# Performance work log

Hardware: AMD Instinct MI355X
Metric: run time of the kernel (lower is better)

The kernel has to match this reference:

```python
import jax, jax.numpy as jnp
import numpy as np
jax.config.update("jax_enable_x64", True)

TAPS, DELAY = 5, 3
EPS = 1e-6        # DNN_WPE.eps: power clamp before WPE
WPE_EPS = 1e-10   # wpe_one_iteration eps: inverse-power clamp + diag loading


def _signal_framing(Y, L):
    # Y: (..., T) -> (..., T-L+1, L) sliding frames (as_strided equivalent)
    T = Y.shape[-1]
    idx = jnp.arange(T - L + 1)[:, None] + jnp.arange(L)[None, :]
    return Y[..., idx]


def _wpe_one_iteration(Y, power, taps, delay):
    # Y: (B,F,C,T) complex128, power: (B,F,T) float64
    B, F, C, T = Y.shape
    inv_power = 1.0 / jnp.maximum(power, WPE_EPS)
    Tp = T - delay - taps + 1
    # tap-stacked delayed signal, taps axis reversed: (B,F,C,Tp,taps)
    Psi = _signal_framing(Y, taps)[..., :Tp, :][..., ::-1]
    Psi_n = Psi.conj() * inv_power[:, :, None, delay + taps - 1:, None]
    # covariance R: (B,F,taps*C,taps*C); cross-corr P: (B,F,taps,C_e,C_d)
    R = jnp.einsum("bfdtk,bfetl->bfkdle", Psi_n, Psi).reshape(B, F, taps * C, taps * C)
    P = jnp.einsum("bfdtk,bfet->bfked", Psi_n, Y[..., delay + taps - 1:])
    # v: (B,F,C_e,taps*C_d); conj filter G = inv(R) @ v^T  (X = v @ inv(R)^T)
    v = P.transpose(0, 1, 3, 2, 4).reshape(B, F, C, taps * C)
    eye = jnp.eye(taps * C, dtype=R.dtype)
    tr = jnp.trace(R, axis1=-2, axis2=-1).real[..., None, None] / (taps * C)
    G = jnp.linalg.solve(R + WPE_EPS * tr * eye, v.transpose(0, 1, 3, 2))
    G = G.reshape(B, F, taps, C, C)  # (B,F,tau,d,e) conjugated filter matrix
    # reverb tail: sum over taps of filtered, delayed signal
    tail = jnp.zeros_like(Y)
    for tau in range(taps):  # taps=5, small fixed loop
        s = delay + tau
        contrib = jnp.einsum("bfde,bfdt->bfet", G[:, :, tau], Y[..., : T - s])
        tail = tail.at[..., s:].add(contrib)
    return Y - tail


def setup_inputs() -> dict:
    key = jax.random.key(0)
    k1, k2, k3 = jax.random.split(key, 3)
    B, T, C, F = 4, 512, 8, 257
    data_real = jax.random.normal(k1, (B, T, C, F), dtype=jnp.float32)
    data_imag = jax.random.normal(k2, (B, T, C, F), dtype=jnp.float32)
    ilens = jax.random.randint(k3, (B,), 256, T + 1)
    return {"data_real": data_real, "data_imag": data_imag, "ilens": ilens}


def reference(data_real, data_imag, ilens):
    # (B,T,C,F) -> (B,F,C,T)
    data = (data_real + 1j * data_imag).transpose(0, 3, 2, 1)
    # power averaged over channels, clamped (B,F,T)
    power = jnp.maximum(jnp.mean(data.real ** 2 + data.imag ** 2, axis=-2), EPS)
    enh = _wpe_one_iteration(data.astype(jnp.complex128), power.astype(jnp.float64), TAPS, DELAY)
    enh = enh.astype(jnp.complex64)
    T = enh.shape[-1]
    pad = (jnp.arange(T)[None, :] >= ilens[:, None])[:, None, None, :]  # (B,1,1,T)
    enh = jnp.where(pad, 0.0 + 0.0j, enh)
    enh = enh.transpose(0, 3, 2, 1)  # back to (B,T,C,F)
    return enh.real, enh.imag, power
```

## Files before the change

kernel.cpp:

```cpp
#include <hip/hip_runtime.h>
#include <hip/hip_fp16.h>

#define B_ 4
#define T_ 512
#define C_ 8
#define F_ 257
#define TAPS 5
#define DELAY 3
#define N_ 40
#define NA 48
#define TP 505
#define T0 7
#define BF (B_*F_)
#define BTCF ((size_t)B_*T_*C_*F_)
#define YSH 532
#define YPAD 8
#define ZSD 20

typedef _Float16 half8 __attribute__((ext_vector_type(8)));
typedef float floatx4 __attribute__((ext_vector_type(4)));
typedef uint32_t uint32x4 __attribute__((ext_vector_type(4)));

__device__ inline uint32_t h2mul(uint32_t a, uint32_t b) {
    __half2 r = __hmul2(__builtin_bit_cast(__half2, a), __builtin_bit_cast(__half2, b));
    return __builtin_bit_cast(uint32_t, r);
}
__device__ inline uint32_t packf16(float2 v) {
    __half2 h = __floats2half2_rn(v.x, v.y);
    return __builtin_bit_cast(uint32_t, h);
}
__device__ inline float2 unpackf16(uint32_t u) {
    __half2 h = __builtin_bit_cast(__half2, u);
    return make_float2(__low2float(h), __high2float(h));
}
__device__ inline half8 mkfrag(uint32_t a, uint32_t b, uint32_t c, uint32_t d) {
    uint32x4 v = {a, b, c, d};
    return __builtin_bit_cast(half8, v);
}
__device__ inline int rowoff(int i) {
    return i * 49 - ((i * (i - 1)) >> 1);
}
__device__ inline int swz_w(int bid) {
    int xcd = bid & 7, slot = bid >> 3;
    return (xcd < 4) ? xcd * 129 + slot : 516 + (xcd - 4) * 128 + slot;
}

struct Frag { half8 X; half8 Y; };

__device__ inline Frag build2(const uint32_t* p, uint32_t sw0, uint32_t sw1,
                              uint32_t sw2, uint32_t sw3) {
    uint32_t q0 = p[0], q1 = p[1], q2 = p[2], q3 = p[3];
    uint32_t q4 = p[4], q5 = p[5], q6 = p[6], q7 = p[7];
    uint32_t x0 = __builtin_amdgcn_perm(q1, q0, 0x05040100);
    uint32_t y0 = __builtin_amdgcn_perm(q1, q0, 0x07060302);
    uint32_t x1 = __builtin_amdgcn_perm(q3, q2, 0x05040100);
    uint32_t y1 = __builtin_amdgcn_perm(q3, q2, 0x07060302);
    uint32_t x2 = __builtin_amdgcn_perm(q5, q4, 0x05040100);
    uint32_t y2 = __builtin_amdgcn_perm(q5, q4, 0x07060302);
    uint32_t x3 = __builtin_amdgcn_perm(q7, q6, 0x05040100);
    uint32_t y3 = __builtin_amdgcn_perm(q7, q6, 0x07060302);
    Frag f;
    f.X = mkfrag(h2mul(x0, sw0), h2mul(x1, sw1), h2mul(x2, sw2), h2mul(x3, sw3));
    f.Y = mkfrag(h2mul(y0, sw0), h2mul(y1, sw1), h2mul(y2, sw2), h2mul(y3, sw3));
    return f;
}
__device__ inline int zs_off(int j) {
    return (j < N_) ? (j & 7) * YSH + (YPAD + 4 - (j >> 3)) : (j - N_) * YSH + (YPAD + T0);
}

__global__ __launch_bounds__(256) void k_stage(const float* __restrict__ in_re,
                                               const float* __restrict__ in_im,
                                               uint32_t* __restrict__ Yh) {
    __shared__ uint32_t tile[32][33];
    int ft = blockIdx.x % 9;
    int tt = blockIdx.x / 9;
    int c = blockIdx.y, b = blockIdx.z;
    int tx = threadIdx.x, ty = threadIdx.y;
    int f = ft * 32 + tx;
#pragma unroll
    for (int i = 0; i < 4; ++i) {
        int t = tt * 32 + ty + i * 8;
        if (f < F_) {
            size_t idx = ((size_t)(b * T_ + t) * C_ + c) * F_ + f;
            tile[ty + i * 8][tx] = packf16(make_float2(in_re[idx], in_im[idx]));
        }
    }
    __syncthreads();
    int t2 = tt * 32 + tx;
#pragma unroll
    for (int i = 0; i < 4; ++i) {
        int f2 = ft * 32 + ty + i * 8;
        if (f2 < F_) {
            Yh[((size_t)(b * F_ + f2) * C_ + c) * T_ + t2] = tile[tx][ty + i * 8];
        }
    }
}

__global__ __launch_bounds__(256) void k_gramsolve(const uint32_t* __restrict__ Yh,
                                                   float2* __restrict__ Gbuf,
                                                   float* __restrict__ pow_out) {
    __shared__ uint32_t sYh[C_ * YSH];
    __shared__ __align__(16) uint32_t pool[3256];
    float* sPow = (float*)pool;
    uint32_t* sw_pk = pool + 640;
    float2* sAugU = (float2*)(pool + 896);
    int tid = threadIdx.x;

    int w = swz_w(blockIdx.x);

    {
        const uint32_t* ys = Yh + (size_t)w * (C_ * T_);
#pragma unroll 4
        for (int k = 0; k < 16; ++k) {
            int idx = tid + k * 256;
            int c = idx >> 9, t = idx & 511;
            sYh[c * YSH + YPAD + t] = ys[idx];
        }
        if (tid < 20) {
            int z = (tid < 8) ? tid : (512 + tid);
#pragma unroll
            for (int c = 0; c < C_; ++c) sYh[c * YSH + z] = 0;
        }
    }
    __syncthreads();

    {
        int t0 = tid, t1 = tid + 256;
        float s0 = 0.f, s1 = 0.f;
#pragma unroll
        for (int c = 0; c < C_; ++c) {
            float2 a0 = unpackf16(sYh[c * YSH + YPAD + t0]);
            float2 a1 = unpackf16(sYh[c * YSH + YPAD + t1]);
            s0 += a0.x * a0.x + a0.y * a0.y;
            s1 += a1.x * a1.x + a1.y * a1.y;
        }
        s0 = fmaxf(s0 * (1.0f / C_), 1e-6f);
        s1 = fmaxf(s1 * (1.0f / C_), 1e-6f);
        pow_out[(size_t)w * T_ + t0] = s0;
        pow_out[(size_t)w * T_ + t1] = s1;
        sPow[t0] = s0;
        sPow[t1] = s1;
    }
    __syncthreads();

    {
        int k0 = 2 * tid, k1 = k0 + 1;
        float w0 = (k0 < TP) ? rsqrtf(sPow[k0 + T0]) : 0.f;
        float w1 = (k1 < TP) ? rsqrtf(sPow[k1 + T0]) : 0.f;
        sw_pk[tid] = packf16(make_float2(w0, w1));
    }
    __syncthreads();

    int wv = tid >> 6, ln = tid & 63;
    int kg = ln >> 4;
    if (wv < 3) {
        int r16 = ln & 15;
        int offB = zs_off(wv * 16 + r16);
#pragma unroll 1
        for (int mt = 0; mt < 3; ++mt) {
            int offA = zs_off(mt * 16 + r16);
            floatx4 aRe = {0.f, 0.f, 0.f, 0.f};
            floatx4 aIm = {0.f, 0.f, 0.f, 0.f};
#pragma unroll 2
            for (int ks = 0; ks < 16; ++ks) {
                int kbase = ks * 32 + kg * 8;
                uint32x4 sv = *(const uint32x4*)&sw_pk[kbase >> 1];
                Frag B = build2(&sYh[offB + kbase], sv[0], sv[1], sv[2], sv[3]);
                Frag A = build2(&sYh[offA + kbase], sv[0], sv[1], sv[2], sv[3]);
                half8 nYa = -A.Y;
                aRe = __builtin_amdgcn_mfma_f32_16x16x32_f16(A.X, B.X, aRe, 0, 0, 0);
                aRe = __builtin_amdgcn_mfma_f32_16x16x32_f16(A.Y, B.Y, aRe, 0, 0, 0);
                aIm = __builtin_amdgcn_mfma_f32_16x16x32_f16(A.X, B.Y, aIm, 0, 0, 0);
                aIm = __builtin_amdgcn_mfma_f32_16x16x32_f16(nYa, B.X, aIm, 0, 0, 0);
            }
#pragma unroll
            for (int r = 0; r < 4; ++r) {
                int m = mt * 16 + kg * 4 + r;
                int col = wv * 16 + r16;
                if (m < N_ && col >= m)
                    sAugU[rowoff(m) + col - m] = make_float2(aRe[r], aIm[r]);
            }
        }
    }
    __syncthreads();

    if (tid < 64) {
        float dv = (tid < N_) ? sAugU[rowoff(tid)].x : 0.f;
#pragma unroll
        for (int off = 32; off; off >>= 1) dv += __shfl_xor(dv, off, 64);
        if (tid < N_) sAugU[rowoff(tid)].x += 1e-10f * dv / N_;
    }
    __syncthreads();

    {
        int ri = tid >> 4, ci = tid & 15;
        float2 dq0, dq1, dq2;
#pragma unroll 1
        for (int p = 0; p < N_ - 2; p += 2) {
            if (p > 0 && ri == 0) {
                int qm = p - 1, roqm = rowoff(qm);
                if (ci < NA - qm)      sAugU[roqm + ci] = dq0;
                if (ci + 16 < NA - qm) sAugU[roqm + ci + 16] = dq1;
                if (ci + 32 < NA - qm) sAugU[roqm + ci + 32] = dq2;
            }
            int q = p + 1;
            int rop = rowoff(p), roq = rowoff(q);
            float2 Upp = sAugU[rop];
            float2 Upq = sAugU[rop + 1];
            float2 Uqq = sAugU[roq];
            float dn0 = Upp.x * Upp.x + Upp.y * Upp.y;
            float i0x = Upp.x / dn0, i0y = -Upp.y / dn0;
            float mqx = Upq.x * i0x + Upq.y * i0y;
            float mqy = Upq.x * i0y - Upq.y * i0x;
            float d1x = Uqq.x - (mqx * Upq.x - mqy * Upq.y);
            float d1y = Uqq.y - (mqx * Upq.y + mqy * Upq.x);
            float dn1 = d1x * d1x + d1y * d1y;
            float i1x = d1x / dn1, i1y = -d1y / dn1;
#pragma unroll 1
            for (int i = q + ri; i < N_; i += 16) {
                if (i == q) {
#pragma unroll
                    for (int s = 0; s < 3; ++s) {
                        int j = q + ci + 16 * s;
                        float2 r = make_float2(0.f, 0.f);
                        if (j < NA) {
                            float2 Upj = sAugU[rop + j - p];
                            float2 Uqj = sAugU[roq + j - q];
                            r.x = Uqj.x - (mqx * Upj.x - mqy * Upj.y);
                            r.y = Uqj.y - (mqx * Upj.y + mqy * Upj.x);
                        }
                        if (s == 0) dq0 = r; else if (s == 1) dq1 = r; else dq2 = r;
                    }
                } else {
                    float2 Upi = sAugU[rop + i - p];
                    float m0x = Upi.x * i0x + Upi.y * i0y;
                    float m0y = Upi.x * i0y - Upi.y * i0x;
                    float2 Uqi = sAugU[roq + i - q];
                    float ax = Uqi.x - (m0x * Upq.x - m0y * Upq.y);
                    float ay = -Uqi.y - (m0x * Upq.y + m0y * Upq.x);
                    float m1x = ax * i1x - ay * i1y;
                    float m1y = ax * i1y + ay * i1x;
                    int roi = rowoff(i) - i;
#pragma unroll 1
                    for (int j = i + ci; j < NA; j += 16) {
                        float2 Upj = sAugU[rop + j - p];
                        float2 Uqj = sAugU[roq + j - q];
                        float u1x = Uqj.x - (mqx * Upj.x - mqy * Upj.y);
                        float u1y = Uqj.y - (mqx * Upj.y + mqy * Upj.x);
                        float2 v = sAugU[roi + j];
                        v.x -= (m0x * Upj.x - m0y * Upj.y) + (m1x * u1x - m1y * u1y);
                        v.y -= (m0x * Upj.y + m0y * Upj.x) + (m1x * u1y + m1y * u1x);
                        sAugU[roi + j] = v;
                    }
                }
            }
            __syncthreads();
        }
        {
            int p = N_ - 2;
            if (ri == 0) {
                int qm = p - 1, roqm = rowoff(qm);
                if (ci < NA - qm)      sAugU[roqm + ci] = dq0;
                if (ci + 16 < NA - qm) sAugU[roqm + ci + 16] = dq1;
                if (ci + 32 < NA - qm) sAugU[roqm + ci + 32] = dq2;
            }
            int rop = rowoff(p);
            float2 piv = sAugU[rop];
            float dn = piv.x * piv.x + piv.y * piv.y;
            float px = piv.x / dn, py = -piv.y / dn;
#pragma unroll 1
            for (int i = p + 1 + ri; i < N_; i += 16) {
                float2 api = sAugU[rop + i - p];
                float mx = api.x * px + api.y * py;
                float my = api.x * py - api.y * px;
                int roi = rowoff(i) - i;
#pragma unroll 1
                for (int j = i + ci; j < NA; j += 16) {
                    float2 apj = sAugU[rop + j - p];
                    float2 v = sAugU[roi + j];
                    v.x -= mx * apj.x - my * apj.y;
                    v.y -= mx * apj.y + my * apj.x;
                    sAugU[roi + j] = v;
                }
            }
            __syncthreads();
        }
    }
    {
        int bc = tid & 7, br = tid >> 3;
        float2 defv = make_float2(0.f, 0.f);
        int defRow = -1;
#pragma unroll 1
        for (int p = N_ - 1; p >= 3; p -= 2) {
            if (defRow >= 0 && br == (defRow & 31))
                sAugU[rowoff(defRow) + N_ + bc - defRow] = defv;
            int q = p - 1;
            int rop = rowoff(p), roq = rowoff(q);
            float2 pivP = sAugU[rop];
            float dnP = pivP.x * pivP.x + pivP.y * pivP.y;
            float pPx = pivP.x / dnP, pPy = -pivP.y / dnP;
            float2 rhsP = sAugU[rop + N_ + bc - p];
            float xPx = rhsP.x * pPx - rhsP.y * pPy;
            float xPy = rhsP.x * pPy + rhsP.y * pPx;
            float2 pivQ = sAugU[roq];
            float dnQ = pivQ.x * pivQ.x + pivQ.y * pivQ.y;
            float pQx = pivQ.x / dnQ, pQy = -pivQ.y / dnQ;
            float2 Uqp = sAugU[roq + 1];
            float2 rhsQ = sAugU[roq + N_ + bc - q];
            float rqx = rhsQ.x - (Uqp.x * xPx - Uqp.y * xPy);
            float rqy = rhsQ.y - (Uqp.x * xPy + Uqp.y * xPx);
            float xQx = rqx * pQx - rqy * pQy;
            float xQy = rqx * pQy + rqy * pQx;
#pragma unroll 1
            for (int i = br; i <= p - 2; i += 32) {
                int roi = rowoff(i) - i;
                float2 Uip = sAugU[roi + p];
                float2 Uiq = sAugU[roi + q];
                float2 v = sAugU[roi + N_ + bc];
                v.x -= (Uip.x * xPx - Uip.y * xPy) + (Uiq.x * xQx - Uiq.y * xQy);
                v.y -= (Uip.x * xPy + Uip.y * xPx) + (Uiq.x * xQy + Uiq.y * xQx);
                sAugU[roi + N_ + bc] = v;
            }
            if (br == (q & 31)) defv = make_float2(rqx, rqy);
            defRow = q;
            __syncthreads();
        }
        {
            if (defRow >= 0 && br == (defRow & 31))
                sAugU[rowoff(defRow) + N_ + bc - defRow] = defv;
            int rop = rowoff(1);
            float2 piv = sAugU[rop];
            float dn = piv.x * piv.x + piv.y * piv.y;
            float px = piv.x / dn, py = -piv.y / dn;
            float2 rhs = sAugU[rop + N_ + bc - 1];
            float xr = rhs.x * px - rhs.y * py;
            float xi = rhs.x * py + rhs.y * px;
            if (br == 0) {
                float2 aip = sAugU[1];
                float2 v = sAugU[N_ + bc];
                v.x -= aip.x * xr - aip.y * xi;
                v.y -= aip.x * xi + aip.y * xr;
                sAugU[N_ + bc] = v;
            }
            __syncthreads();
        }
    }
    for (int idx = tid; idx < N_ * C_; idx += 256) {
        int j = idx >> 3;
        int e = idx & 7;
        int roj = rowoff(j);
        float2 piv = sAugU[roj];
        float dnm = piv.x * piv.x + piv.y * piv.y;
        float pix = piv.x / dnm, piy = -piv.y / dnm;
        float2 rhs = sAugU[roj + N_ + e - j];
        Gbuf[(size_t)w * (N_ * C_) + idx] =
            make_float2(rhs.x * pix - rhs.y * piy, rhs.x * piy + rhs.y * pix);
    }
}

__global__ __launch_bounds__(256) void k_tail(const uint32_t* __restrict__ Yh,
                                              const float2* __restrict__ Gbuf,
                                              const int* __restrict__ ilens,
                                              float* __restrict__ out_re,
                                              float* __restrict__ out_im) {
    __shared__ __align__(16) uint32_t zRe[64 * ZSD];
    __shared__ __align__(16) uint32_t zIm[64 * ZSD];
    int w = swz_w(blockIdx.x);
    int half = blockIdx.y;
    int b = w / F_;
    int f = w - b * F_;
    int ilen = ilens[b];
    const uint32_t* yw = Yh + (size_t)w * (C_ * T_);
    const float2* gw = Gbuf + (size_t)w * (N_ * C_);
    int tid = threadIdx.x;
    int wv = tid >> 6, ln = tid & 63, kg = ln >> 4;

    half8 aFr[2], aFi[2];
    {
        int m = ln & 15;
#pragma unroll
        for (int ks = 0; ks < 2; ++ks) {
            half8 hr = {}, hi = {};
#pragma unroll
            for (int q = 0; q < 8; ++q) {
                int j = ks * 32 + kg * 8 + q;
                float gx = 0.f, gy = 0.f;
                if (m < 8 && j < N_) {
                    float2 g = gw[j * 8 + m];
                    gx = g.x; gy = g.y;
                }
                hr[q] = (_Float16)gx;
                hi[q] = (_Float16)gy;
            }
            aFr[ks] = hr;
            aFi[ks] = hi;
        }
    }

    int trow = wv * 16 + (ln & 15);
#pragma unroll 1
    for (int ch = 0; ch < 4; ++ch) {
        int c0 = half * 256 + ch * 64;
        for (int idx = tid; idx < 1280; idx += 256) {
            int jp = idx >> 6, tl = idx & 63;
            int j0 = 2 * jp, j1 = j0 + 1;
            int s0 = c0 + tl - 3 - (j0 >> 3);
            uint32_t y0 = 0, y1 = 0;
            if (s0 >= 0) {
                y0 = yw[(j0 & 7) * T_ + s0];
                y1 = yw[(j1 & 7) * T_ + s0];
            }
            zRe[tl * ZSD + jp] = __builtin_amdgcn_perm(y1, y0, 0x05040100);
            zIm[tl * ZSD + jp] = __builtin_amdgcn_perm(y1, y0, 0x07060302);
        }
        __syncthreads();
        floatx4 accR = {0.f, 0.f, 0.f, 0.f};
        floatx4 accI = {0.f, 0.f, 0.f, 0.f};
        {
            int o0 = trow * ZSD + kg * 4;
            half8 Br0 = __builtin_bit_cast(half8, *(const uint32x4*)&zRe[o0]);
            half8 Bi0 = __builtin_bit_cast(half8, *(const uint32x4*)&zIm[o0]);
            half8 Br1 = {}, Bi1 = {};
            if (kg == 0) {
                int o1 = trow * ZSD + 16;
                Br1 = __builtin_bit_cast(half8, *(const uint32x4*)&zRe[o1]);
                Bi1 = __builtin_bit_cast(half8, *(const uint32x4*)&zIm[o1]);
            }
            half8 nFi0 = -aFi[0], nFi1 = -aFi[1];
            accR = __builtin_amdgcn_mfma_f32_16x16x32_f16(aFr[0], Br0, accR, 0, 0, 0);
            accR = __builtin_amdgcn_mfma_f32_16x16x32_f16(aFr[1], Br1, accR, 0, 0, 0);
            accI = __builtin_amdgcn_mfma_f32_16x16x32_f16(aFi[0], Br0, accI, 0, 0, 0);
            accI = __builtin_amdgcn_mfma_f32_16x16x32_f16(aFi[1], Br1, accI, 0, 0, 0);
            accR = __builtin_amdgcn_mfma_f32_16x16x32_f16(nFi0, Bi0, accR, 0, 0, 0);
            accR = __builtin_amdgcn_mfma_f32_16x16x32_f16(nFi1, Bi1, accR, 0, 0, 0);
            accI = __builtin_amdgcn_mfma_f32_16x16x32_f16(aFr[0], Bi0, accI, 0, 0, 0);
            accI = __builtin_amdgcn_mfma_f32_16x16x32_f16(aFr[1], Bi1, accI, 0, 0, 0);
        }
        if (kg < 2) {
            int tg = c0 + trow;
            bool dead = (tg >= ilen);
#pragma unroll
            for (int r = 0; r < 4; ++r) {
                int e = kg * 4 + r;
                float2 cf = unpackf16(yw[e * T_ + tg]);
                float ex = cf.x - accR[r];
                float ey = cf.y - accI[r];
                if (dead) { ex = 0.f; ey = 0.f; }
                size_t o = (size_t)b * T_ * C_ * F_ + ((size_t)tg * C_ + e) * F_ + f;
                out_re[o] = ex;
                out_im[o] = ey;
            }
        }
        __syncthreads();
    }
}

extern "C" void kernel_launch(void* const* d_in, const int* in_sizes, int n_in,
                              void* d_out, int out_size, void* d_ws, size_t ws_size,
                              hipStream_t stream) {
    const float* in_re = (const float*)d_in[0];
    const float* in_im = (const float*)d_in[1];
    const int* ilens = (const int*)d_in[2];

    float* out_re = (float*)d_out;
    float* out_im = out_re + BTCF;
    float* out_pw = out_im + BTCF;

    uint32_t* Yh = (uint32_t*)d_ws;
    float2* Gbuf = (float2*)(Yh + (size_t)BF * C_ * T_);

    dim3 tb(32, 8);
    dim3 tg(9 * 16, C_, B_);
    k_stage<<<tg, tb, 0, stream>>>(in_re, in_im, Yh);
    k_gramsolve<<<BF, 256, 0, stream>>>(Yh, Gbuf, out_pw);
    k_tail<<<dim3(BF, 2), 256, 0, stream>>>(Yh, Gbuf, ilens, out_re, out_im);
}
```

Before: 221.1 us.

## Fuse gram/solve and tail kernels into one per-bin kernel with staged K-slices

Merges the gram+solve kernel and the tail-filter kernel into a single kernel per (batch,freq) bin, keeping the solved filter in shared memory instead of round-tripping through a global buffer. The Gram matrix build is restructured: instead of caching the whole 8x512 signal in LDS and re-permuting fragments per MFMA, it stages pre-weighted, de-interleaved X/Y fragments for 128-sample slices into LDS, then runs all three row tiles per wave with register accumulators. This cuts LDS footprint, a kernel launch and the G buffer traffic. In exchange, the tail stage loses its 2-way split across blocks, so each block does twice the tail work serially and parallelism halves for that phase.

```diff
diff --git a/kernel.cpp b/kernel.cpp
--- a/kernel.cpp
+++ b/kernel.cpp
@@ -13,9 +13,8 @@
 #define T0 7
 #define BF (B_*F_)
 #define BTCF ((size_t)B_*T_*C_*F_)
-#define YSH 532
-#define YPAD 8
 #define ZSD 20
+#define PRS 68
 
 typedef _Float16 half8 __attribute__((ext_vector_type(8)));
 typedef float floatx4 __attribute__((ext_vector_type(4)));
@@ -33,39 +32,12 @@
     __half2 h = __builtin_bit_cast(__half2, u);
     return make_float2(__low2float(h), __high2float(h));
 }
-__device__ inline half8 mkfrag(uint32_t a, uint32_t b, uint32_t c, uint32_t d) {
-    uint32x4 v = {a, b, c, d};
-    return __builtin_bit_cast(half8, v);
-}
 __device__ inline int rowoff(int i) {
     return i * 49 - ((i * (i - 1)) >> 1);
 }
 __device__ inline int swz_w(int bid) {
     int xcd = bid & 7, slot = bid >> 3;
     return (xcd < 4) ? xcd * 129 + slot : 516 + (xcd - 4) * 128 + slot;
-}
-
-struct Frag { half8 X; half8 Y; };
-
-__device__ inline Frag build2(const uint32_t* p, uint32_t sw0, uint32_t sw1,
-                              uint32_t sw2, uint32_t sw3) {
-    uint32_t q0 = p[0], q1 = p[1], q2 = p[2], q3 = p[3];
-    uint32_t q4 = p[4], q5 = p[5], q6 = p[6], q7 = p[7];
-    uint32_t x0 = __builtin_amdgcn_perm(q1, q0, 0x05040100);
-    uint32_t y0 = __builtin_amdgcn_perm(q1, q0, 0x07060302);
-    uint32_t x1 = __builtin_amdgcn_perm(q3, q2, 0x05040100);
-    uint32_t y1 = __builtin_amdgcn_perm(q3, q2, 0x07060302);
-    uint32_t x2 = __builtin_amdgcn_perm(q5, q4, 0x05040100);
-    uint32_t y2 = __builtin_amdgcn_perm(q5, q4, 0x07060302);
-    uint32_t x3 = __builtin_amdgcn_perm(q7, q6, 0x05040100);
-    uint32_t y3 = __builtin_amdgcn_perm(q7, q6, 0x07060302);
-    Frag f;
-    f.X = mkfrag(h2mul(x0, sw0), h2mul(x1, sw1), h2mul(x2, sw2), h2mul(x3, sw3));
-    f.Y = mkfrag(h2mul(y0, sw0), h2mul(y1, sw1), h2mul(y2, sw2), h2mul(y3, sw3));
-    return f;
-}
-__device__ inline int zs_off(int j) {
-    return (j < N_) ? (j & 7) * YSH + (YPAD + 4 - (j >> 3)) : (j - N_) * YSH + (YPAD + T0);
 }
 
 __global__ __launch_bounds__(256) void k_stage(const float* __restrict__ in_re,
@@ -96,41 +68,34 @@
     }
 }
 
-__global__ __launch_bounds__(256) void k_gramsolve(const uint32_t* __restrict__ Yh,
-                                                   float2* __restrict__ Gbuf,
-                                                   float* __restrict__ pow_out) {
-    __shared__ uint32_t sYh[C_ * YSH];
-    __shared__ __align__(16) uint32_t pool[3256];
+__global__ __launch_bounds__(256) void k_compute(const uint32_t* __restrict__ Yh,
+                                                 const int* __restrict__ ilens,
+                                                 float* __restrict__ out_re,
+                                                 float* __restrict__ out_im,
+                                                 float* __restrict__ pow_out) {
+    __shared__ __align__(16) uint32_t pool[7296];
     float* sPow = (float*)pool;
-    uint32_t* sw_pk = pool + 640;
-    float2* sAugU = (float2*)(pool + 896);
+    uint32_t* sw_pk = pool + 512;
+    uint32_t* zX = pool + 768;
+    uint32_t* zY = pool + 768 + 48 * PRS;
+    float2* sAugU = (float2*)(pool + 768);
+    uint32_t* zRe = pool + 4032;
+    uint32_t* zIm = pool + 4032 + 64 * ZSD;
     int tid = threadIdx.x;
 
     int w = swz_w(blockIdx.x);
-
-    {
-        const uint32_t* ys = Yh + (size_t)w * (C_ * T_);
-#pragma unroll 4
-        for (int k = 0; k < 16; ++k) {
-            int idx = tid + k * 256;
-            int c = idx >> 9, t = idx & 511;
-            sYh[c * YSH + YPAD + t] = ys[idx];
-        }
-        if (tid < 20) {
-            int z = (tid < 8) ? tid : (512 + tid);
-#pragma unroll
-            for (int c = 0; c < C_; ++c) sYh[c * YSH + z] = 0;
-        }
-    }
-    __syncthreads();
+    int b = w / F_;
+    int f = w - b * F_;
+    int ilen = ilens[b];
+    const uint32_t* yw = Yh + (size_t)w * (C_ * T_);
 
     {
         int t0 = tid, t1 = tid + 256;
         float s0 = 0.f, s1 = 0.f;
 #pragma unroll
         for (int c = 0; c < C_; ++c) {
-            float2 a0 = unpackf16(sYh[c * YSH + YPAD + t0]);
-            float2 a1 = unpackf16(sYh[c * YSH + YPAD + t1]);
+            float2 a0 = unpackf16(yw[c * T_ + t0]);
+            float2 a1 = unpackf16(yw[c * T_ + t1]);
             s0 += a0.x * a0.x + a0.y * a0.y;
             s1 += a1.x * a1.x + a1.y * a1.y;
         }
@@ -152,34 +117,99 @@
     __syncthreads();
 
     int wv = tid >> 6, ln = tid & 63;
-    int kg = ln >> 4;
+    int kg = ln >> 4, r16 = ln & 15;
+    floatx4 aRe0 = {0.f, 0.f, 0.f, 0.f}, aIm0 = {0.f, 0.f, 0.f, 0.f};
+    floatx4 aRe1 = {0.f, 0.f, 0.f, 0.f}, aIm1 = {0.f, 0.f, 0.f, 0.f};
+    floatx4 aRe2 = {0.f, 0.f, 0.f, 0.f}, aIm2 = {0.f, 0.f, 0.f, 0.f};
+#pragma unroll 1
+    for (int sl = 0; sl < 4; ++sl) {
+#pragma unroll
+        for (int rep = 0; rep < 3; ++rep) {
+            int task = tid + rep * 256;
+            int j = task >> 4, g = task & 15;
+            int c = (j < N_) ? (j & 7) : (j - N_);
+            int sh = (j < N_) ? (4 - (j >> 3)) : 7;
+            int base = sl * 128 + g * 8 + sh;
+            const uint32_t* yc = yw + c * T_;
+            uint32_t q0 = yc[(base + 0 < 512) ? base + 0 : 511];
+            uint32_t q1 = yc[(base + 1 < 512) ? base + 1 : 511];
+            uint32_t q2 = yc[(base + 2 < 512) ? base + 2 : 511];
+            uint32_t q3 = yc[(base + 3 < 512) ? base + 3 : 511];
+            uint32_t q4 = yc[(base + 4 < 512) ? base + 4 : 511];
+            uint32_t q5 = yc[(base + 5 < 512) ? base + 5 : 511];
+            uint32_t q6 = yc[(base + 6 < 512) ? base + 6 : 511];
+            uint32_t q7 = yc[(base + 7 < 512) ? base + 7 : 511];
+            uint32x4 sv = *(const uint32x4*)&sw_pk[(sl * 128 + g * 8) >> 1];
+            uint32_t x0 = __builtin_amdgcn_perm(q1, q0, 0x05040100);
+            uint32_t y0 = __builtin_amdgcn_perm(q1, q0, 0x07060302);
+            uint32_t x1 = __builtin_amdgcn_perm(q3, q2, 0x05040100);
+            uint32_t y1 = __builtin_amdgcn_perm(q3, q2, 0x07060302);
+            uint32_t x2 = __builtin_amdgcn_perm(q5, q4, 0x05040100);
+            uint32_t y2 = __builtin_amdgcn_perm(q5, q4, 0x07060302);
+            uint32_t x3 = __builtin_amdgcn_perm(q7, q6, 0x05040100);
+            uint32_t y3 = __builtin_amdgcn_perm(q7, q6, 0x07060302);
+            uint32x4 vx = {h2mul(x0, sv[0]), h2mul(x1, sv[1]),
+                           h2mul(x2, sv[2]), h2mul(x3, sv[3])};
+            uint32x4 vy = {h2mul(y0, sv[0]), h2mul(y1, sv[1]),
+                           h2mul(y2, sv[2]), h2mul(y3, sv[3])};
+            *(uint32x4*)&zX[j * PRS + g * 4] = vx;
+            *(uint32x4*)&zY[j * PRS + g * 4] = vy;
+        }
+        __syncthreads();
+        if (wv < 3) {
+            int rowB = wv * 16 + r16;
+#pragma unroll
+            for (int l = 0; l < 4; ++l) {
+                int off = l * 16 + kg * 4;
+                half8 BX = __builtin_bit_cast(half8, *(const uint32x4*)&zX[rowB * PRS + off]);
+                half8 BY = __builtin_bit_cast(half8, *(const uint32x4*)&zY[rowB * PRS + off]);
+                {
+                    half8 AX = __builtin_bit_cast(half8, *(const uint32x4*)&zX[r16 * PRS + off]);
+                    half8 AY = __builtin_bit_cast(half8, *(const uint32x4*)&zY[r16 * PRS + off]);
+                    half8 nAY = -AY;
+                    aRe0 = __builtin_amdgcn_mfma_f32_16x16x32_f16(AX, BX, aRe0, 0, 0, 0);
+                    aRe0 = __builtin_amdgcn_mfma_f32_16x16x32_f16(AY, BY, aRe0, 0, 0, 0);
+                    aIm0 = __builtin_amdgcn_mfma_f32_16x16x32_f16(AX, BY, aIm0, 0, 0, 0);
+                    aIm0 = __builtin_amdgcn_mfma_f32_16x16x32_f16(nAY, BX, aIm0, 0, 0, 0);
+                }
+                {
+                    half8 AX = __builtin_bit_cast(half8, *(const uint32x4*)&zX[(16 + r16) * PRS + off]);
+                    half8 AY = __builtin_bit_cast(half8, *(const uint32x4*)&zY[(16 + r16) * PRS + off]);
+                    half8 nAY = -AY;
+                    aRe1 = __builtin_amdgcn_mfma_f32_16x16x32_f16(AX, BX, aRe1, 0, 0, 0);
+                    aRe1 = __builtin_amdgcn_mfma_f32_16x16x32_f16(AY, BY, aRe1, 0, 0, 0);
+                    aIm1 = __builtin_amdgcn_mfma_f32_16x16x32_f16(AX, BY, aIm1, 0, 0, 0);
+                    aIm1 = __builtin_amdgcn_mfma_f32_16x16x32_f16(nAY, BX, aIm1, 0, 0, 0);
+                }
+                {
+                    half8 AX = __builtin_bit_cast(half8, *(const uint32x4*)&zX[(32 + r16) * PRS + off]);
+                    half8 AY = __builtin_bit_cast(half8, *(const uint32x4*)&zY[(32 + r16) * PRS + off]);
+                    half8 nAY = -AY;
+                    aRe2 = __builtin_amdgcn_mfma_f32_16x16x32_f16(AX, BX, aRe2, 0, 0, 0);
+                    aRe2 = __builtin_amdgcn_mfma_f32_16x16x32_f16(AY, BY, aRe2, 0, 0, 0);
+                    aIm2 = __builtin_amdgcn_mfma_f32_16x16x32_f16(AX, BY, aIm2, 0, 0, 0);
+                    aIm2 = __builtin_amdgcn_mfma_f32_16x16x32_f16(nAY, BX, aIm2, 0, 0, 0);
+                }
+            }
+        }
+        __syncthreads();
+    }
     if (wv < 3) {
-        int r16 = ln & 15;
-        int offB = zs_off(wv * 16 + r16);
-#pragma unroll 1
-        for (int mt = 0; mt < 3; ++mt) {
-            int offA = zs_off(mt * 16 + r16);
-            floatx4 aRe = {0.f, 0.f, 0.f, 0.f};
-            floatx4 aIm = {0.f, 0.f, 0.f, 0.f};
-#pragma unroll 2
-            for (int ks = 0; ks < 16; ++ks) {
-                int kbase = ks * 32 + kg * 8;
-                uint32x4 sv = *(const uint32x4*)&sw_pk[kbase >> 1];
-                Frag B = build2(&sYh[offB + kbase], sv[0], sv[1], sv[2], sv[3]);
-                Frag A = build2(&sYh[offA + kbase], sv[0], sv[1], sv[2], sv[3]);
-                half8 nYa = -A.Y;
-                aRe = __builtin_amdgcn_mfma_f32_16x16x32_f16(A.X, B.X, aRe, 0, 0, 0);
-                aRe = __builtin_amdgcn_mfma_f32_16x16x32_f16(A.Y, B.Y, aRe, 0, 0, 0);
-                aIm = __builtin_amdgcn_mfma_f32_16x16x32_f16(A.X, B.Y, aIm, 0, 0, 0);
-                aIm = __builtin_amdgcn_mfma_f32_16x16x32_f16(nYa, B.X, aIm, 0, 0, 0);
-            }
-#pragma unroll
-            for (int r = 0; r < 4; ++r) {
-                int m = mt * 16 + kg * 4 + r;
-                int col = wv * 16 + r16;
-                if (m < N_ && col >= m)
-                    sAugU[rowoff(m) + col - m] = make_float2(aRe[r], aIm[r]);
-            }
+        int col = wv * 16 + r16;
+#pragma unroll
+        for (int r = 0; r < 4; ++r) {
+            int m = kg * 4 + r;
+            if (col >= m) sAugU[rowoff(m) + col - m] = make_float2(aRe0[r], aIm0[r]);
+        }
+#pragma unroll
+        for (int r = 0; r < 4; ++r) {
+            int m = 16 + kg * 4 + r;
+            if (col >= m) sAugU[rowoff(m) + col - m] = make_float2(aRe1[r], aIm1[r]);
+        }
+#pragma unroll
+        for (int r = 0; r < 4; ++r) {
+            int m = 32 + kg * 4 + r;
+            if (m < N_ && col >= m) sAugU[rowoff(m) + col - m] = make_float2(aRe2[r], aIm2[r]);
         }
     }
     __syncthreads();
@@ -353,31 +383,14 @@
         float dnm = piv.x * piv.x + piv.y * piv.y;
         float pix = piv.x / dnm, piy = -piv.y / dnm;
         float2 rhs = sAugU[roj + N_ + e - j];
-        Gbuf[(size_t)w * (N_ * C_) + idx] =
+        sAugU[roj + N_ + e - j] =
             make_float2(rhs.x * pix - rhs.y * piy, rhs.x * piy + rhs.y * pix);
     }
-}
-
-__global__ __launch_bounds__(256) void k_tail(const uint32_t* __restrict__ Yh,
-                                              const float2* __restrict__ Gbuf,
-                                              const int* __restrict__ ilens,
-                                              float* __restrict__ out_re,
-                                              float* __restrict__ out_im) {
-    __shared__ __align__(16) uint32_t zRe[64 * ZSD];
-    __shared__ __align__(16) uint32_t zIm[64 * ZSD];
-    int w = swz_w(blockIdx.x);
-    int half = blockIdx.y;
-    int b = w / F_;
-    int f = w - b * F_;
-    int ilen = ilens[b];
-    const uint32_t* yw = Yh + (size_t)w * (C_ * T_);
-    const float2* gw = Gbuf + (size_t)w * (N_ * C_);
-    int tid = threadIdx.x;
-    int wv = tid >> 6, ln = tid & 63, kg = ln >> 4;
+    __syncthreads();
 
     half8 aFr[2], aFi[2];
     {
-        int m = ln & 15;
+        int m = r16;
 #pragma unroll
         for (int ks = 0; ks < 2; ++ks) {
             half8 hr = {}, hi = {};
@@ -386,7 +399,7 @@
                 int j = ks * 32 + kg * 8 + q;
                 float gx = 0.f, gy = 0.f;
                 if (m < 8 && j < N_) {
-                    float2 g = gw[j * 8 + m];
+                    float2 g = sAugU[rowoff(j) + N_ + m - j];
                     gx = g.x; gy = g.y;
                 }
                 hr[q] = (_Float16)gx;
@@ -396,11 +409,12 @@
             aFi[ks] = hi;
         }
     }
-
-    int trow = wv * 16 + (ln & 15);
-#pragma unroll 1
-    for (int ch = 0; ch < 4; ++ch) {
-        int c0 = half * 256 + ch * 64;
+    __syncthreads();
+
+    int trow = wv * 16 + r16;
+#pragma unroll 1
+    for (int ch = 0; ch < 8; ++ch) {
+        int c0 = ch * 64;
         for (int idx = tid; idx < 1280; idx += 256) {
             int jp = idx >> 6, tl = idx & 63;
             int j0 = 2 * jp, j1 = j0 + 1;
@@ -467,11 +481,9 @@
     float* out_pw = out_im + BTCF;
 
     uint32_t* Yh = (uint32_t*)d_ws;
-    float2* Gbuf = (float2*)(Yh + (size_t)BF * C_ * T_);
 
     dim3 tb(32, 8);
     dim3 tg(9 * 16, C_, B_);
     k_stage<<<tg, tb, 0, stream>>>(in_re, in_im, Yh);
-    k_gramsolve<<<BF, 256, 0, stream>>>(Yh, Gbuf, out_pw);
-    k_tail<<<dim3(BF, 2), 256, 0, stream>>>(Yh, Gbuf, ilens, out_re, out_im);
-}
+    k_compute<<<BF, 256, 0, stream>>>(Yh, ilens, out_re, out_im, out_pw);
+}
```

Measured after the change: 222.3 us. Within noise of the previous version (+0.5%).
